# Performance work log

Hardware: AMD Instinct MI355X
Metric: run time of the kernel (lower is better)

## Reference

```python
import jax, jax.numpy as jnp
import numpy as np

NUM_THING = 80
THING_STUFF_IDS = np.concatenate([np.arange(80), np.arange(80, 133)])  # thing_class_ids + stuff_class_ids
H_OUT, W_OUT = 641, 641
PIXEL_CONF_THR = 0.4
CLASS_CONF_THR = 0.7
NEG = -1e9  # mask value standing in for removing undetected slots


def _resize_bilinear_align_corners(x, h_out, w_out):
    # x: [h_in, w_in, C]; tf.compat.v1.image.resize_bilinear(..., align_corners=True)
    h_in, w_in = x.shape[0], x.shape[1]
    ys = jnp.linspace(0.0, h_in - 1.0, h_out)
    xs = jnp.linspace(0.0, w_in - 1.0, w_out)
    y0 = jnp.floor(ys).astype(jnp.int32)
    x0 = jnp.floor(xs).astype(jnp.int32)
    y1 = jnp.minimum(y0 + 1, h_in - 1)
    x1 = jnp.minimum(x0 + 1, w_in - 1)
    wy = (ys - y0.astype(ys.dtype))[:, None, None]
    wx = (xs - x0.astype(xs.dtype))[None, :, None]
    rows = x[y0] * (1.0 - wy) + x[y1] * wy          # [h_out, w_in, C]
    return rows[:, x0] * (1.0 - wx) + rows[:, x1] * wx  # [h_out, w_out, C]


def setup_inputs() -> dict:
    key = jax.random.key(0)
    k1, k2 = jax.random.split(key)
    pixel_space_mask_logits = jax.random.normal(k1, (161, 161, 128), dtype=jnp.float32)
    transformer_class_probs = jax.random.uniform(k2, (128, 134), dtype=jnp.float32)
    return {"pixel_space_mask_logits": pixel_space_mask_logits,
            "transformer_class_probs": transformer_class_probs}


def reference(pixel_space_mask_logits, transformer_class_probs):
    # --- _get_transformer_class_prediction (void channel dropped first) ---
    probs = transformer_class_probs[:, :-1]                     # [M, C]
    cls_pred = jnp.argmax(probs, axis=-1).astype(jnp.float32)   # [M]
    cls_conf = jnp.max(probs, axis=-1)                          # [M]
    detected = cls_conf >= CLASS_CONF_THR                       # [M] bool
    num_detections = jnp.sum(detected.astype(jnp.int32))
    # index of each detected slot within the detected subset (matches tf.gather order)
    det_subset_index = jnp.cumsum(detected.astype(jnp.int32)) - 1  # [M]

    # --- resize logits to full image (pieces=1 -> single full-width piece) ---
    resized = _resize_bilinear_align_corners(pixel_space_mask_logits, H_OUT, W_OUT)  # [H, W, M]

    # mask out undetected slots instead of gathering (same math, static shape)
    masked = jnp.where(detected[None, None, :], resized, NEG)   # [H, W, M]

    full_max = jnp.max(resized, axis=-1)                        # [H, W]
    det_max = jnp.max(masked, axis=-1)                          # [H, W]
    detected_pixel = (full_max == det_max).astype(jnp.float32)

    pixel_conf = jnp.max(jax.nn.softmax(masked, axis=-1), axis=-1)
    confident_region = (pixel_conf > PIXEL_CONF_THR).astype(jnp.float32) * detected_pixel

    argmax_slot = jnp.argmax(masked, axis=-1)                   # [H, W] slot index
    mask_id_map = det_subset_index[argmax_slot]                 # index within detected subset
    sem_float = cls_pred[argmax_slot]                           # detected_mask_class_pred gathered

    thing_mask = (sem_float < NUM_THING).astype(jnp.float32) * confident_region
    stuff_mask = (sem_float >= NUM_THING).astype(jnp.float32) * confident_region
    semantic_map = jnp.asarray(THING_STUFF_IDS, jnp.int32)[jnp.round(sem_float).astype(jnp.int32)]
    mask_id_map_plus_one = mask_id_map.astype(jnp.int32) + 1

    # --- empty-detection branch (tf.cond) expressed as select ---
    has_det = num_detections > 0
    mask_id_map_plus_one = jnp.where(has_det, mask_id_map_plus_one, jnp.ones_like(mask_id_map_plus_one))
    semantic_map = jnp.where(has_det, semantic_map, jnp.zeros_like(semantic_map))
    thing_mask = jnp.where(has_det, thing_mask, jnp.zeros_like(thing_mask))
    stuff_mask = jnp.where(has_det, stuff_mask, jnp.zeros_like(stuff_mask))
    return (mask_id_map_plus_one, semantic_map, thing_mask, stuff_mask)
```

## Files before the change

### kernel.cpp

```cpp
#include <hip/hip_runtime.h>

#pragma clang fp contract(off)

#define NP 410881

__global__ __launch_bounds__(1024) void slot_kernel(
    const float* __restrict__ probs, float* __restrict__ cls_pred,
    int* __restrict__ det_idx, unsigned long long* __restrict__ det_mask,
    int* __restrict__ num_det) {
  __shared__ float s_val[128];
  __shared__ int s_arg[128];
  __shared__ int s_tot0;
  int tid = threadIdx.x;
  int wv = tid >> 6, lane = tid & 63;

  float bvv[8];
  int bii[8];
#pragma unroll
  for (int k = 0; k < 8; ++k) {
    int r = wv * 8 + k;
    const float* row = probs + r * 134;
    float v0 = row[lane];
    float v1 = row[lane + 64];
    float v2 = (lane < 5) ? row[lane + 128] : -1.0f;
    float bv = v0;
    int bi = lane;
    if (v1 > bv) { bv = v1; bi = lane + 64; }
    if (v2 > bv) { bv = v2; bi = lane + 128; }
    bvv[k] = bv; bii[k] = bi;
  }
#pragma unroll
  for (int k = 0; k < 8; ++k) {
    float bv = bvv[k];
    int bi = bii[k];
#pragma unroll
    for (int off = 32; off; off >>= 1) {
      float ov = __shfl_xor(bv, off);
      int oi = __shfl_xor(bi, off);
      if (ov > bv || (ov == bv && oi < bi)) { bv = ov; bi = oi; }
    }
    if (lane == 0) { s_val[wv * 8 + k] = bv; s_arg[wv * 8 + k] = bi; }
  }
  __syncthreads();

  bool flag = false;
  unsigned long long b = 0;
  if (tid < 128) flag = s_val[tid] >= 0.7f;
  if (wv < 2) b = __ballot(flag);
  if (tid < 128 && lane == 0) {
    det_mask[wv] = b;
    if (wv == 0) s_tot0 = __popcll(b);
  }
  __syncthreads();
  if (tid < 128) {
    int incl = __popcll(b & ((1ull << lane) - 1)) + (flag ? 1 : 0) +
               (wv ? s_tot0 : 0);
    det_idx[tid] = incl - 1;
    cls_pred[tid] = (float)s_arg[tid];
    if (tid == 127) *num_det = incl;
  }
}

__global__ __launch_bounds__(128) void post_kernel(
    const float* __restrict__ logits, const float* __restrict__ ws_cls,
    const int* __restrict__ ws_didx,
    const unsigned long long* __restrict__ ws_mask,
    const int* __restrict__ ws_ndet, float* __restrict__ out) {
#pragma clang fp contract(off)
  int tid = threadIdx.x;
  int X0 = blockIdx.x << 4, Y0 = blockIdx.y << 4;

  int strip = tid & 7, py = tid >> 3;
  int cx = strip >> 1, h = strip & 1;
  int cy = py >> 2;
  int xa = X0 + (cx << 2) + (h << 1);
  int y = Y0 + py;

  int ndet = *ws_ndet;
  if (ndet == 0) {
    if (y < 641) {
      if (xa < 641) {
        int i0 = y * 641 + xa;
        out[i0] = 1.0f; out[NP + i0] = 0.f; out[2 * NP + i0] = 0.f; out[3 * NP + i0] = 0.f;
      }
      if (xa + 1 < 641) {
        int i1 = y * 641 + xa + 1;
        out[i1] = 1.0f; out[NP + i1] = 0.f; out[2 * NP + i1] = 0.f; out[3 * NP + i1] = 0.f;
      }
    }
    return;
  }

  int tx0 = min((X0 >> 2) + cx, 160);
  int tx1 = min(tx0 + 1, 160);
  int ty0 = min((Y0 >> 2) + cy, 160);
  int ty1 = min(ty0 + 1, 160);
  const float* P00 = logits + ((ty0 * 161 + tx0) << 7);
  const float* P01 = logits + ((ty0 * 161 + tx1) << 7);
  const float* P10 = logits + ((ty1 * 161 + tx0) << 7);
  const float* P11 = logits + ((ty1 * 161 + tx1) << 7);

  float wy = 0.25f * (float)(py & 3);
  float iwy = 1.0f - wy;
  float wx0 = 0.5f * (float)h;
  float wx1 = wx0 + 0.25f;
  float iwx0 = 1.0f - wx0, iwx1 = 1.0f - wx1;

  float m0 = -INFINITY, m1 = -INFINITY;
  int am0 = 0, am1 = 0;
  float T0 = 0.f, T1 = 0.f;
  bool dp0 = true, dp1 = true;

  if (ndet == 128) {
    float ms0[4], ms1[4], Ts0[4], Ts1[4];
    int as0[4], as1[4];
#pragma unroll
    for (int j = 0; j < 4; ++j) {
      ms0[j] = -INFINITY; ms1[j] = -INFINITY;
      Ts0[j] = 0.f; Ts1[j] = 0.f;
      as0[j] = 0; as1[j] = 0;
    }
#define CH(A00, A01, A10, A11, CIDX, J)                                        \
  {                                                                            \
    float r0 = (A00) * iwy + (A10) * wy;                                       \
    float r1 = (A01) * iwy + (A11) * wy;                                       \
    float v0 = r0 * iwx0 + r1 * wx0;                                           \
    float v1 = r0 * iwx1 + r1 * wx1;                                           \
    bool g0 = v0 > ms0[J]; ms0[J] = g0 ? v0 : ms0[J]; as0[J] = g0 ? (CIDX) : as0[J]; \
    bool g1 = v1 > ms1[J]; ms1[J] = g1 ? v1 : ms1[J]; as1[J] = g1 ? (CIDX) : as1[J]; \
    Ts0[J] += __expf(v0);                                                      \
    Ts1[J] += __expf(v1);                                                      \
  }
#pragma unroll 4
    for (int c = 0; c < 128; c += 4) {
      float4 q00 = *(const float4*)(P00 + c);
      float4 q01 = *(const float4*)(P01 + c);
      float4 q10 = *(const float4*)(P10 + c);
      float4 q11 = *(const float4*)(P11 + c);
      CH(q00.x, q01.x, q10.x, q11.x, c + 0, 0);
      CH(q00.y, q01.y, q10.y, q11.y, c + 1, 1);
      CH(q00.z, q01.z, q10.z, q11.z, c + 2, 2);
      CH(q00.w, q01.w, q10.w, q11.w, c + 3, 3);
    }
#undef CH
    m0 = ms0[0]; am0 = as0[0]; m1 = ms1[0]; am1 = as1[0];
#pragma unroll
    for (int j = 1; j < 4; ++j) {
      if (ms0[j] > m0 || (ms0[j] == m0 && as0[j] < am0)) { m0 = ms0[j]; am0 = as0[j]; }
      if (ms1[j] > m1 || (ms1[j] == m1 && as1[j] < am1)) { m1 = ms1[j]; am1 = as1[j]; }
    }
    T0 = (Ts0[0] + Ts0[1]) + (Ts0[2] + Ts0[3]);
    T1 = (Ts1[0] + Ts1[1]) + (Ts1[2] + Ts1[3]);
  } else {
    unsigned long long mlo = ws_mask[0], mhi = ws_mask[1];
    float rm0 = -INFINITY, rm1 = -INFINITY;
#pragma unroll 4
    for (int c = 0; c < 128; ++c) {
      float a00 = P00[c], a01 = P01[c];
      float a10 = P10[c], a11 = P11[c];
      float r0 = a00 * iwy + a10 * wy;
      float r1 = a01 * iwy + a11 * wy;
      float v0 = r0 * iwx0 + r1 * wx0;
      float v1 = r0 * iwx1 + r1 * wx1;
      rm0 = fmaxf(rm0, v0);
      rm1 = fmaxf(rm1, v1);
      unsigned long long bit = (c < 64) ? (mlo >> c) : (mhi >> (c - 64));
      if (bit & 1) {
        bool g0 = v0 > m0; m0 = g0 ? v0 : m0; am0 = g0 ? c : am0;
        bool g1 = v1 > m1; m1 = g1 ? v1 : m1; am1 = g1 ? c : am1;
        T0 += __expf(v0);
        T1 += __expf(v1);
      }
    }
    dp0 = (rm0 == m0);
    dp1 = (rm1 == m1);
  }

  float cg0 = ((__expf(m0) > 0.4f * T0) && dp0) ? 1.0f : 0.0f;
  float cg1 = ((__expf(m1) > 0.4f * T1) && dp1) ? 1.0f : 0.0f;
  float sem0 = ws_cls[am0], sem1 = ws_cls[am1];
  float mid0 = (float)(ws_didx[am0] + 1), mid1 = (float)(ws_didx[am1] + 1);
  float th0 = (sem0 < 80.f) ? cg0 : 0.f;
  float st0 = cg0 - th0;
  float th1 = (sem1 < 80.f) ? cg1 : 0.f;
  float st1 = cg1 - th1;

  if (y < 641) {
    if (xa < 641) {
      int i0 = y * 641 + xa;
      out[i0] = mid0; out[NP + i0] = sem0; out[2 * NP + i0] = th0; out[3 * NP + i0] = st0;
    }
    if (xa + 1 < 641) {
      int i1 = y * 641 + xa + 1;
      out[i1] = mid1; out[NP + i1] = sem1; out[2 * NP + i1] = th1; out[3 * NP + i1] = st1;
    }
  }
}

extern "C" void kernel_launch(void* const* d_in, const int* in_sizes, int n_in,
                              void* d_out, int out_size, void* d_ws,
                              size_t ws_size, hipStream_t stream) {
  const float* logits = (const float*)d_in[0];
  const float* probs = (const float*)d_in[1];
  float* out = (float*)d_out;

  float* ws_f = (float*)d_ws;
  float* cls_pred = ws_f;
  int* det_idx = (int*)(ws_f + 128);
  unsigned long long* det_mask = (unsigned long long*)(ws_f + 256);
  int* num_det = (int*)(ws_f + 260);

  slot_kernel<<<1, 1024, 0, stream>>>(probs, cls_pred, det_idx, det_mask,
                                      num_det);

  dim3 grid(41, 41);
  post_kernel<<<grid, 128, 0, stream>>>(logits, cls_pred, det_idx, det_mask,
                                        num_det, out);
}
```

Baseline: 106.0 us.

## Split channel reduction across two thread halves with shared-memory combine

The post kernel now uses 512 threads per 16x16 tile: each pixel gets two threads, each reducing 64 of the 128 slot channels, and the partial max/argmax/exp-sum results are merged through shared memory. Before, 128 threads each handled two adjacent pixels over all 128 channels. This raises parallelism and shortens each thread's serial loop, giving more latency hiding for the gather loads. In exchange it adds a block barrier, shared-memory traffic, and drops the reuse where two pixels shared the same four corner loads, so each corner value is now loaded twice as often per output.

```diff
diff --git a/kernel.cpp b/kernel.cpp
--- a/kernel.cpp
+++ b/kernel.cpp
@@ -61,138 +61,115 @@
   }
 }
 
-__global__ __launch_bounds__(128) void post_kernel(
+__global__ __launch_bounds__(512) void post_kernel(
     const float* __restrict__ logits, const float* __restrict__ ws_cls,
     const int* __restrict__ ws_didx,
     const unsigned long long* __restrict__ ws_mask,
     const int* __restrict__ ws_ndet, float* __restrict__ out) {
 #pragma clang fp contract(off)
-  int tid = threadIdx.x;
+  __shared__ float sm[256], sT[256], srm[256];
+  __shared__ int sa[256];
+
+  int t = threadIdx.x;
+  int p = t & 255;
+  int half = t >> 8;
   int X0 = blockIdx.x << 4, Y0 = blockIdx.y << 4;
-
-  int strip = tid & 7, py = tid >> 3;
-  int cx = strip >> 1, h = strip & 1;
-  int cy = py >> 2;
-  int xa = X0 + (cx << 2) + (h << 1);
-  int y = Y0 + py;
+  int x = X0 + (p & 15);
+  int y = Y0 + (p >> 4);
+  bool valid = (x < 641) && (y < 641);
+  int xc = min(x, 640), yc = min(y, 640);
 
   int ndet = *ws_ndet;
   if (ndet == 0) {
-    if (y < 641) {
-      if (xa < 641) {
-        int i0 = y * 641 + xa;
-        out[i0] = 1.0f; out[NP + i0] = 0.f; out[2 * NP + i0] = 0.f; out[3 * NP + i0] = 0.f;
-      }
-      if (xa + 1 < 641) {
-        int i1 = y * 641 + xa + 1;
-        out[i1] = 1.0f; out[NP + i1] = 0.f; out[2 * NP + i1] = 0.f; out[3 * NP + i1] = 0.f;
-      }
+    if (valid && half == 0) {
+      int i0 = y * 641 + x;
+      out[i0] = 1.0f; out[NP + i0] = 0.f; out[2 * NP + i0] = 0.f; out[3 * NP + i0] = 0.f;
     }
     return;
   }
 
-  int tx0 = min((X0 >> 2) + cx, 160);
-  int tx1 = min(tx0 + 1, 160);
-  int ty0 = min((Y0 >> 2) + cy, 160);
-  int ty1 = min(ty0 + 1, 160);
-  const float* P00 = logits + ((ty0 * 161 + tx0) << 7);
-  const float* P01 = logits + ((ty0 * 161 + tx1) << 7);
-  const float* P10 = logits + ((ty1 * 161 + tx0) << 7);
-  const float* P11 = logits + ((ty1 * 161 + tx1) << 7);
+  int tx0 = xc >> 2, ty0 = yc >> 2;
+  int tx1 = min(tx0 + 1, 160), ty1 = min(ty0 + 1, 160);
+  float wx = 0.25f * (float)(xc & 3), iwx = 1.0f - wx;
+  float wy = 0.25f * (float)(yc & 3), iwy = 1.0f - wy;
 
-  float wy = 0.25f * (float)(py & 3);
-  float iwy = 1.0f - wy;
-  float wx0 = 0.5f * (float)h;
-  float wx1 = wx0 + 0.25f;
-  float iwx0 = 1.0f - wx0, iwx1 = 1.0f - wx1;
+  int co = half << 6;
+  const float* P00 = logits + ((ty0 * 161 + tx0) << 7) + co;
+  const float* P01 = logits + ((ty0 * 161 + tx1) << 7) + co;
+  const float* P10 = logits + ((ty1 * 161 + tx0) << 7) + co;
+  const float* P11 = logits + ((ty1 * 161 + tx1) << 7) + co;
 
-  float m0 = -INFINITY, m1 = -INFINITY;
-  int am0 = 0, am1 = 0;
-  float T0 = 0.f, T1 = 0.f;
-  bool dp0 = true, dp1 = true;
+  float m = -INFINITY;
+  int am = 0;
+  float T = 0.f;
+  float rm = -INFINITY;
 
   if (ndet == 128) {
-    float ms0[4], ms1[4], Ts0[4], Ts1[4];
-    int as0[4], as1[4];
+    float ms[4], Ts[4];
+    int as[4];
 #pragma unroll
-    for (int j = 0; j < 4; ++j) {
-      ms0[j] = -INFINITY; ms1[j] = -INFINITY;
-      Ts0[j] = 0.f; Ts1[j] = 0.f;
-      as0[j] = 0; as1[j] = 0;
-    }
+    for (int j = 0; j < 4; ++j) { ms[j] = -INFINITY; Ts[j] = 0.f; as[j] = 0; }
 #define CH(A00, A01, A10, A11, CIDX, J)                                        \
   {                                                                            \
     float r0 = (A00) * iwy + (A10) * wy;                                       \
     float r1 = (A01) * iwy + (A11) * wy;                                       \
-    float v0 = r0 * iwx0 + r1 * wx0;                                           \
-    float v1 = r0 * iwx1 + r1 * wx1;                                           \
-    bool g0 = v0 > ms0[J]; ms0[J] = g0 ? v0 : ms0[J]; as0[J] = g0 ? (CIDX) : as0[J]; \
-    bool g1 = v1 > ms1[J]; ms1[J] = g1 ? v1 : ms1[J]; as1[J] = g1 ? (CIDX) : as1[J]; \
-    Ts0[J] += __expf(v0);                                                      \
-    Ts1[J] += __expf(v1);                                                      \
+    float v = r0 * iwx + r1 * wx;                                              \
+    bool g = v > ms[J]; ms[J] = g ? v : ms[J]; as[J] = g ? (CIDX) : as[J];     \
+    Ts[J] += __expf(v);                                                        \
   }
-#pragma unroll 4
-    for (int c = 0; c < 128; c += 4) {
+#pragma unroll 2
+    for (int c = 0; c < 64; c += 4) {
       float4 q00 = *(const float4*)(P00 + c);
       float4 q01 = *(const float4*)(P01 + c);
       float4 q10 = *(const float4*)(P10 + c);
       float4 q11 = *(const float4*)(P11 + c);
-      CH(q00.x, q01.x, q10.x, q11.x, c + 0, 0);
-      CH(q00.y, q01.y, q10.y, q11.y, c + 1, 1);
-      CH(q00.z, q01.z, q10.z, q11.z, c + 2, 2);
-      CH(q00.w, q01.w, q10.w, q11.w, c + 3, 3);
+      CH(q00.x, q01.x, q10.x, q11.x, co + c + 0, 0);
+      CH(q00.y, q01.y, q10.y, q11.y, co + c + 1, 1);
+      CH(q00.z, q01.z, q10.z, q11.z, co + c + 2, 2);
+      CH(q00.w, q01.w, q10.w, q11.w, co + c + 3, 3);
     }
 #undef CH
-    m0 = ms0[0]; am0 = as0[0]; m1 = ms1[0]; am1 = as1[0];
+    m = ms[0]; am = as[0];
 #pragma unroll
-    for (int j = 1; j < 4; ++j) {
-      if (ms0[j] > m0 || (ms0[j] == m0 && as0[j] < am0)) { m0 = ms0[j]; am0 = as0[j]; }
-      if (ms1[j] > m1 || (ms1[j] == m1 && as1[j] < am1)) { m1 = ms1[j]; am1 = as1[j]; }
-    }
-    T0 = (Ts0[0] + Ts0[1]) + (Ts0[2] + Ts0[3]);
-    T1 = (Ts1[0] + Ts1[1]) + (Ts1[2] + Ts1[3]);
+    for (int j = 1; j < 4; ++j)
+      if (ms[j] > m || (ms[j] == m && as[j] < am)) { m = ms[j]; am = as[j]; }
+    T = (Ts[0] + Ts[1]) + (Ts[2] + Ts[3]);
+    rm = m;
   } else {
-    unsigned long long mlo = ws_mask[0], mhi = ws_mask[1];
-    float rm0 = -INFINITY, rm1 = -INFINITY;
+    unsigned long long msk = ws_mask[half];
 #pragma unroll 4
-    for (int c = 0; c < 128; ++c) {
+    for (int c = 0; c < 64; ++c) {
       float a00 = P00[c], a01 = P01[c];
       float a10 = P10[c], a11 = P11[c];
       float r0 = a00 * iwy + a10 * wy;
       float r1 = a01 * iwy + a11 * wy;
-      float v0 = r0 * iwx0 + r1 * wx0;
-      float v1 = r0 * iwx1 + r1 * wx1;
-      rm0 = fmaxf(rm0, v0);
-      rm1 = fmaxf(rm1, v1);
-      unsigned long long bit = (c < 64) ? (mlo >> c) : (mhi >> (c - 64));
-      if (bit & 1) {
-        bool g0 = v0 > m0; m0 = g0 ? v0 : m0; am0 = g0 ? c : am0;
-        bool g1 = v1 > m1; m1 = g1 ? v1 : m1; am1 = g1 ? c : am1;
-        T0 += __expf(v0);
-        T1 += __expf(v1);
+      float v = r0 * iwx + r1 * wx;
+      rm = fmaxf(rm, v);
+      if ((msk >> c) & 1) {
+        bool g = v > m; m = g ? v : m; am = g ? (co + c) : am;
+        T += __expf(v);
       }
     }
-    dp0 = (rm0 == m0);
-    dp1 = (rm1 == m1);
   }
 
-  float cg0 = ((__expf(m0) > 0.4f * T0) && dp0) ? 1.0f : 0.0f;
-  float cg1 = ((__expf(m1) > 0.4f * T1) && dp1) ? 1.0f : 0.0f;
-  float sem0 = ws_cls[am0], sem1 = ws_cls[am1];
-  float mid0 = (float)(ws_didx[am0] + 1), mid1 = (float)(ws_didx[am1] + 1);
-  float th0 = (sem0 < 80.f) ? cg0 : 0.f;
-  float st0 = cg0 - th0;
-  float th1 = (sem1 < 80.f) ? cg1 : 0.f;
-  float st1 = cg1 - th1;
+  if (half == 1) { sm[p] = m; sa[p] = am; sT[p] = T; srm[p] = rm; }
+  __syncthreads();
+  if (half == 0) {
+    float m1 = sm[p], T1 = sT[p], rm1 = srm[p];
+    int a1 = sa[p];
+    if (m1 > m || (m1 == m && a1 < am)) { m = m1; am = a1; }
+    T += T1;
+    rm = fmaxf(rm, rm1);
+    bool dp = (rm == m);
 
-  if (y < 641) {
-    if (xa < 641) {
-      int i0 = y * 641 + xa;
-      out[i0] = mid0; out[NP + i0] = sem0; out[2 * NP + i0] = th0; out[3 * NP + i0] = st0;
-    }
-    if (xa + 1 < 641) {
-      int i1 = y * 641 + xa + 1;
-      out[i1] = mid1; out[NP + i1] = sem1; out[2 * NP + i1] = th1; out[3 * NP + i1] = st1;
+    float cg = ((__expf(m) > 0.4f * T) && dp) ? 1.0f : 0.0f;
+    float sem = ws_cls[am];
+    float mid = (float)(ws_didx[am] + 1);
+    float th = (sem < 80.f) ? cg : 0.f;
+    float st = cg - th;
+    if (valid) {
+      int i0 = y * 641 + x;
+      out[i0] = mid; out[NP + i0] = sem; out[2 * NP + i0] = th; out[3 * NP + i0] = st;
     }
   }
 }
@@ -214,6 +191,6 @@
                                       num_det);
 
   dim3 grid(41, 41);
-  post_kernel<<<grid, 128, 0, stream>>>(logits, cls_pred, det_idx, det_mask,
+  post_kernel<<<grid, 512, 0, stream>>>(logits, cls_pred, det_idx, det_mask,
                                         num_det, out);
 }
```

New measurement: 97.50 us. -8.0%, faster.
